# Kernel tuning notes

Measured on AMD Instinct MI355X. Metric: run time of the kernel, lower is better.

Reference implementation:

```python
import jax, jax.numpy as jnp
import numpy as np

N = 100000
IN_C = 256
OUT_C = 128
E = 3200000
NNZ = 3200000
K = 3  # n_wavelets
ATT_H = 64


def spmm(idx, vals, m):
    # idx: [2, nnz] (row, col), vals: [nnz], m: [N, d] -> [N, d]
    rows, cols = idx[0], idx[1]
    return jax.ops.segment_sum(vals[:, None] * m[cols], rows, num_segments=N)


def appnp_k1_a0(h, edge_index):
    # PyG APPNP(K=1, alpha=0) == one gcn-normalized propagation with self-loops
    loops = jnp.arange(N, dtype=edge_index.dtype)
    row = jnp.concatenate([edge_index[0], loops])
    col = jnp.concatenate([edge_index[1], loops])
    ones = jnp.ones(row.shape[0], dtype=h.dtype)
    deg = jax.ops.segment_sum(ones, col, num_segments=N)
    dinv = jnp.where(deg > 0, 1.0 / jnp.sqrt(deg), 0.0)
    norm = dinv[row] * dinv[col]
    return jax.ops.segment_sum(norm[:, None] * h[col], row, num_segments=N)


def setup_inputs() -> dict:
    key = jax.random.key(0)
    ks = jax.random.split(key, 12)
    x = jax.random.normal(ks[0], (N, IN_C), dtype=jnp.float32)
    edge_index = jax.random.randint(ks[1], (2, E), 0, N)
    phi_idx = jax.random.randint(ks[2], (K, 2, NNZ), 0, N)
    phi_vals = jax.random.uniform(ks[3], (K, NNZ), dtype=jnp.float32) * (1.0 / 32.0)
    phi_inv_idx = jax.random.randint(ks[4], (K, 2, NNZ), 0, N)
    phi_inv_vals = jax.random.uniform(ks[5], (K, NNZ), dtype=jnp.float32) * (1.0 / 32.0)
    # learned parameters
    lin_w = jax.random.normal(ks[6], (IN_C, OUT_C), dtype=jnp.float32) * (1.0 / np.sqrt(IN_C))
    lin_b = jnp.zeros((OUT_C,), dtype=jnp.float32)
    gw_w = jax.random.normal(ks[7], (IN_C, OUT_C), dtype=jnp.float32) * (1.0 / np.sqrt(IN_C))
    diag_w = jax.random.uniform(ks[8], (N,), dtype=jnp.float32, minval=0.9, maxval=1.1)
    att_w1 = jax.random.normal(ks[9], (OUT_C, ATT_H), dtype=jnp.float32) * (1.0 / np.sqrt(OUT_C))
    att_b1 = jnp.zeros((ATT_H,), dtype=jnp.float32)
    att_w2 = jax.random.normal(ks[10], (ATT_H, 1), dtype=jnp.float32) * (1.0 / np.sqrt(ATT_H))
    return {"x": x, "edge_index": edge_index, "phi_idx": phi_idx, "phi_vals": phi_vals,
            "phi_inv_idx": phi_inv_idx, "phi_inv_vals": phi_inv_vals,
            "lin_w": lin_w, "lin_b": lin_b, "gw_w": gw_w, "diag_w": diag_w,
            "att_w1": att_w1, "att_b1": att_b1, "att_w2": att_w2}


def reference(x, edge_index, phi_idx, phi_vals, phi_inv_idx, phi_inv_vals,
              lin_w, lin_b, gw_w, diag_w, att_w1, att_b1, att_w2):
    # --- mean branch: Linear -> L2 normalize * 1.8 -> APPNP(K=1, alpha=0)
    mean = x @ lin_w + lin_b
    nrm = jnp.linalg.norm(mean, axis=1, keepdims=True)
    mean = mean / jnp.maximum(nrm, 1e-12) * 1.8
    mean = appnp_k1_a0(mean, edge_index)

    # --- logstd branch: GraphWaveletLayer (activation = identity)
    x_ = x @ gw_w  # [N, OUT_C]
    outs = []
    for i in range(K):
        t = spmm(phi_inv_idx[i], phi_inv_vals[i], x_)
        t = diag_w[:, None] * t
        t = spmm(phi_idx[i], phi_vals[i], t)
        outs.append(t)
    z = jnp.stack(outs, axis=1)  # [N, K, OUT_C]

    # --- attention pooling over wavelet axis
    w = jax.nn.relu(jnp.einsum('nkd,dh->nkh', z, att_w1) + att_b1) @ att_w2  # [N, K, 1]
    beta = jax.nn.softmax(w, axis=1)
    logstd = (beta * z).sum(axis=1)  # [N, OUT_C]
    return (mean, logstd)
```

## Files before the change

kernel.cpp:

```cpp
#include <hip/hip_runtime.h>
#include <hip/hip_bf16.h>
#include <hip/hip_fp16.h>


#define WS_HIST  2
#define WS_BUILD 6
#define WS_GATH  8

__global__ __launch_bounds__(256) void hist_kernel(const int* __restrict__ idx,
                                                   int* __restrict__ cnt, int n) {
    int i = blockIdx.x * 256 + threadIdx.x;
    if (i < n) atomicAdd(&cnt[__builtin_nontemporal_load(idx + i)], 1);
}

__global__ __launch_bounds__(256) void dinv_kernel(int* __restrict__ cnt,
                                                   float* __restrict__ dinv, int n) {
    int i = blockIdx.x * 256 + threadIdx.x;
    if (i < n) { dinv[i] = rsqrtf((float)(cnt[i] + 1)); cnt[i] = 0; }
}

__global__ __launch_bounds__(256) void scan_reduce_kernel(
    const int* __restrict__ cnt, int* __restrict__ bsum, int N) {
    __shared__ int wsum[4];
    int base = blockIdx.x * 1024;
    int t = threadIdx.x;
    int s = 0;
#pragma unroll
    for (int j = 0; j < 4; ++j) {
        int idx = base + t * 4 + j;
        if (idx < N) s += cnt[idx];
    }
#pragma unroll
    for (int off = 32; off; off >>= 1) s += __shfl_xor(s, off);
    int lane = t & 63, w = t >> 6;
    if (lane == 0) wsum[w] = s;
    __syncthreads();
    if (t == 0) bsum[blockIdx.x] = wsum[0] + wsum[1] + wsum[2] + wsum[3];
}

__global__ void scan_bsum_kernel(const int* __restrict__ bsum,
                                 int* __restrict__ bofs,
                                 int* __restrict__ ptr, int nblk, int N) {
    if (threadIdx.x == 0 && blockIdx.x == 0) {
        int run = 0;
        for (int i = 0; i < nblk; ++i) { bofs[i] = run; run += bsum[i]; }
        bofs[nblk] = run;
        ptr[N] = run;
    }
}

__global__ __launch_bounds__(256) void scan_block_kernel(
    int* __restrict__ cnt, const int* __restrict__ bofs,
    int* __restrict__ ptr, int* __restrict__ cursor, int N) {
    __shared__ int wsum[4];
    int base = blockIdx.x * 1024;
    int t = threadIdx.x, lane = t & 63, w = t >> 6;
    int v[4]; int s = 0;
#pragma unroll
    for (int j = 0; j < 4; ++j) {
        int idx = base + t * 4 + j;
        v[j] = (idx < N) ? cnt[idx] : 0;
        s += v[j];
    }
    int incl = s;
#pragma unroll
    for (int off = 1; off < 64; off <<= 1) {
        int nn = __shfl_up(incl, off);
        if (lane >= off) incl += nn;
    }
    if (lane == 63) wsum[w] = incl;
    __syncthreads();
    int wofs = 0;
    for (int i = 0; i < w; ++i) wofs += wsum[i];
    int run = bofs[blockIdx.x] + wofs + incl - s;
#pragma unroll
    for (int j = 0; j < 4; ++j) {
        int idx = base + t * 4 + j;
        if (idx < N) { ptr[idx] = run; cursor[idx] = run; cnt[idx] = 0; }
        run += v[j];
    }
}

__global__ __launch_bounds__(256) void fused_pipe_kernel(
    const int* __restrict__ ptr_g, const int2* __restrict__ cpair_g,
    const __half* __restrict__ src, const float* __restrict__ init_src,
    const float* __restrict__ dinv,
    float* __restrict__ dstf, __half* __restrict__ dsth, int N, int nnz_g,
    const int* __restrict__ rows_b, const int* __restrict__ cols_b,
    const float* __restrict__ vals_b, const float* __restrict__ diag,
    int* __restrict__ cursor_b, unsigned long long* __restrict__ cpair_b,
    int nnz_b, int mode,
    const int* __restrict__ rows_h, int* __restrict__ cnt, int nnz_h,
    int mix)
{
    int role, lid, nloc;
    if (!mix) { role = 2; lid = blockIdx.x; nloc = gridDim.x; }
    else {
        int r = blockIdx.x & 15, g = blockIdx.x >> 4, ng = gridDim.x >> 4;
        if (r < WS_HIST)                { role = 0; lid = g * WS_HIST + r;                nloc = ng * WS_HIST; }
        else if (r < WS_HIST + WS_BUILD){ role = 1; lid = g * WS_BUILD + (r - WS_HIST);   nloc = ng * WS_BUILD; }
        else                            { role = 2; lid = g * WS_GATH + (r - WS_HIST - WS_BUILD); nloc = ng * WS_GATH; }
    }

    if (role == 0) {
        if (!rows_h) return;
        int stride = nloc * 256;
        for (int i = lid * 256 + threadIdx.x; i < nnz_h; i += stride)
            atomicAdd(&cnt[__builtin_nontemporal_load(rows_h + i)], 1);
        return;
    }
    if (role == 1) {
        if (!rows_b) return;
        int stride = nloc * 256;
        for (int i = lid * 256 + threadIdx.x; i < nnz_b; i += stride) {
            int r = __builtin_nontemporal_load(rows_b + i);
            int c = __builtin_nontemporal_load(cols_b + i);
            float v;
            if (mode == 2) v = dinv[r] * dinv[c];
            else {
                v = __builtin_nontemporal_load(vals_b + i);
                if (mode == 1) v *= diag[c];
            }
            int pos = atomicAdd(&cursor_b[r], 1);
            unsigned long long pk =
                ((unsigned long long)(unsigned)__float_as_uint(v) << 32) | (unsigned)c;
            __builtin_nontemporal_store(pk, cpair_b + pos);
        }
        return;
    }

    const int lane = threadIdx.x & 63;
    const size_t lofs = (size_t)(lane * 2);
    int wid = (lid * 256 + threadIdx.x) >> 6;
    const int nwaves = (nloc * 256) >> 6;
    for (int row = wid; row < N; row += nwaves) {
        int s = ptr_g[row], e = ptr_g[row + 1];
        e = min(e, nnz_g); s = max(0, min(s, e));
        float accx = 0.f, accy = 0.f;
        if (init_src) {
            float d = dinv[row];
            float dd = d * d;
            float2 m = *(const float2*)(init_src + (size_t)row * 128 + lofs);
            accx = dd * m.x; accy = dd * m.y;
        }
        for (int base = s; base < e; base += 64) {
            int n = min(64, e - base);
            int2 p = make_int2(0, 0);
            if (lane < n) p = cpair_g[base + lane];
            int j = 0;
            for (; j + 16 <= n; j += 16) {
                __half2 sv[16];
                float vj[16];
#pragma unroll
                for (int u = 0; u < 16; ++u) {
                    int cj = __builtin_amdgcn_readlane(p.x, j + u);
                    vj[u] = __int_as_float(__builtin_amdgcn_readlane(p.y, j + u));
                    sv[u] = *(const __half2*)(src + (size_t)cj * 128 + lofs);
                }
#pragma unroll
                for (int u = 0; u < 16; ++u) {
                    accx += vj[u] * __low2float(sv[u]);
                    accy += vj[u] * __high2float(sv[u]);
                }
            }
            for (; j + 4 <= n; j += 4) {
                __half2 sv[4];
                float vj[4];
#pragma unroll
                for (int u = 0; u < 4; ++u) {
                    int cj = __builtin_amdgcn_readlane(p.x, j + u);
                    vj[u] = __int_as_float(__builtin_amdgcn_readlane(p.y, j + u));
                    sv[u] = *(const __half2*)(src + (size_t)cj * 128 + lofs);
                }
#pragma unroll
                for (int u = 0; u < 4; ++u) {
                    accx += vj[u] * __low2float(sv[u]);
                    accy += vj[u] * __high2float(sv[u]);
                }
            }
            for (; j < n; ++j) {
                int cj = __builtin_amdgcn_readlane(p.x, j);
                float vj = __int_as_float(__builtin_amdgcn_readlane(p.y, j));
                __half2 sv = *(const __half2*)(src + (size_t)cj * 128 + lofs);
                accx += vj * __low2float(sv);
                accy += vj * __high2float(sv);
            }
        }
        if (dstf) {
            float2 o; o.x = accx; o.y = accy;
            *(float2*)(dstf + (size_t)row * 128 + lofs) = o;
        }
        if (dsth) {
            *(__half2*)(dsth + (size_t)row * 128 + lofs) =
                __floats2half2_rn(accx, accy);
        }
    }
}

__global__ __launch_bounds__(256) void gemm_fused(
    const float* __restrict__ x, const float* __restrict__ lin_w,
    const float* __restrict__ lin_b, const float* __restrict__ gw_w,
    float* __restrict__ mean0, __half* __restrict__ xwh, int M) {
    __shared__ float As[32][68];
    __shared__ float Bs[32][64];
    const int tid = threadIdx.x;
    const int tx = tid & 15, ty = tid >> 4;
    const int row0 = blockIdx.x * 64;
    const int nt = blockIdx.y;
    const float* __restrict__ W = (nt < 2) ? lin_w : gw_w;
    const int colbase = (nt & 1) * 64;

    const int ar = tid >> 3;
    const int ac = (tid & 7) << 2;
    const int bk = tid >> 4;
    const int bn = (tid & 15) << 2;

    float acc[4][4] = {};

    for (int kt = 0; kt < 256; kt += 32) {
#pragma unroll
        for (int rr = 0; rr < 2; ++rr) {
            int r = ar + rr * 32;
            int grow = row0 + r;
            float4 v = make_float4(0.f, 0.f, 0.f, 0.f);
            if (grow < M) v = *(const float4*)(x + (size_t)grow * 256 + kt + ac);
            As[ac + 0][r] = v.x; As[ac + 1][r] = v.y;
            As[ac + 2][r] = v.z; As[ac + 3][r] = v.w;
        }
#pragma unroll
        for (int rr = 0; rr < 2; ++rr) {
            int k = bk + rr * 16;
            *(float4*)&Bs[k][bn] =
                *(const float4*)(W + (size_t)(kt + k) * 128 + colbase + bn);
        }
        __syncthreads();
#pragma unroll
        for (int k = 0; k < 32; ++k) {
            float4 a = *(const float4*)&As[k][ty * 4];
            float4 b = *(const float4*)&Bs[k][tx * 4];
            float av[4] = {a.x, a.y, a.z, a.w};
            float bv[4] = {b.x, b.y, b.z, b.w};
#pragma unroll
            for (int i = 0; i < 4; ++i)
#pragma unroll
                for (int j = 0; j < 4; ++j) acc[i][j] += av[i] * bv[j];
        }
        __syncthreads();
    }

    if (nt < 2) {
        float4 bb = *(const float4*)(lin_b + colbase + tx * 4);
#pragma unroll
        for (int i = 0; i < 4; ++i) {
            int grow = row0 + ty * 4 + i;
            if (grow < M) {
                float4 o = make_float4(acc[i][0] + bb.x, acc[i][1] + bb.y,
                                       acc[i][2] + bb.z, acc[i][3] + bb.w);
                *(float4*)(mean0 + (size_t)grow * 128 + colbase + tx * 4) = o;
            }
        }
    } else {
#pragma unroll
        for (int i = 0; i < 4; ++i) {
            int grow = row0 + ty * 4 + i;
            if (grow < M) {
                union { __half2 h[2]; int2 i2; } u;
                u.h[0] = __floats2half2_rn(acc[i][0], acc[i][1]);
                u.h[1] = __floats2half2_rn(acc[i][2], acc[i][3]);
                *(int2*)(xwh + (size_t)grow * 128 + colbase + tx * 4) = u.i2;
            }
        }
    }
}

__global__ __launch_bounds__(256) void rownorm_kernel(float* __restrict__ m,
                                                      __half* __restrict__ mh,
                                                      int n) {
    const int lane = threadIdx.x & 63;
    int wid = (blockIdx.x * 256 + threadIdx.x) >> 6;
    if (wid >= n) return;
    float2 v = *(float2*)(m + (size_t)wid * 128 + lane * 2);
    float ss = v.x * v.x + v.y * v.y;
#pragma unroll
    for (int off = 32; off; off >>= 1) ss += __shfl_xor(ss, off);
    float s = sqrtf(ss);
    float sc = 1.8f / fmaxf(s, 1e-12f);
    v.x *= sc; v.y *= sc;
    *(float2*)(m + (size_t)wid * 128 + lane * 2) = v;
    *(__half2*)(mh + (size_t)wid * 128 + lane * 2) = __floats2half2_rn(v.x, v.y);
}

__global__ __launch_bounds__(256) void attn_h_kernel(
    const __half* __restrict__ z0, const __half* __restrict__ z1,
    const float* __restrict__ z2, const float* __restrict__ w1,
    const float* __restrict__ b1, const float* __restrict__ w2,
    float* __restrict__ out, int n) {
    const int lane = threadIdx.x & 63;
    float w1reg[128];
#pragma unroll
    for (int d = 0; d < 128; ++d) w1reg[d] = w1[d * 64 + lane];
    const float b1l = b1[lane];
    const float w2l = w2[lane];

    int wid = (blockIdx.x * 256 + threadIdx.x) >> 6;
    const int nwaves = (gridDim.x * 256) >> 6;
    for (int node = wid; node < n; node += nwaves) {
        float2 za = __half22float2(*(const __half2*)(z0 + (size_t)node * 128 + lane * 2));
        float2 zb = __half22float2(*(const __half2*)(z1 + (size_t)node * 128 + lane * 2));
        float2 zc = *(const float2*)(z2 + (size_t)node * 128 + lane * 2);
        float wk[3];
#pragma unroll
        for (int k = 0; k < 3; ++k) {
            float zx = (k == 0) ? za.x : (k == 1) ? zb.x : zc.x;
            float zy = (k == 0) ? za.y : (k == 1) ? zb.y : zc.y;
            float acc = 0.f;
#pragma unroll
            for (int d2 = 0; d2 < 64; ++d2) {
                float ze = __uint_as_float(__builtin_amdgcn_readlane(__float_as_uint(zx), d2));
                float zo = __uint_as_float(__builtin_amdgcn_readlane(__float_as_uint(zy), d2));
                acc += ze * w1reg[2 * d2] + zo * w1reg[2 * d2 + 1];
            }
            float h = fmaxf(acc + b1l, 0.f) * w2l;
#pragma unroll
            for (int off = 32; off; off >>= 1) h += __shfl_xor(h, off);
            wk[k] = h;
        }
        float mx = fmaxf(wk[0], fmaxf(wk[1], wk[2]));
        float e0 = __expf(wk[0] - mx);
        float e1 = __expf(wk[1] - mx);
        float e2 = __expf(wk[2] - mx);
        float inv = 1.f / (e0 + e1 + e2);
        float be0 = e0 * inv, be1 = e1 * inv, be2 = e2 * inv;
        float2 o;
        o.x = be0 * za.x + be1 * zb.x + be2 * zc.x;
        o.y = be0 * za.y + be1 * zb.y + be2 * zc.y;
        *(float2*)(out + (size_t)node * 128 + lane * 2) = o;
    }
}

__global__ __launch_bounds__(256) void f2h_kernel(const float* __restrict__ in,
                                                  __half* __restrict__ out,
                                                  size_t n2) {
    size_t i = (size_t)blockIdx.x * 256 + threadIdx.x;
    if (i >= n2) return;
    float2 v = ((const float2*)in)[i];
    ((__half2*)out)[i] = __floats2half2_rn(v.x, v.y);
}

__global__ __launch_bounds__(256) void spmm_h_kernel(
    const int* __restrict__ rows, const int* __restrict__ cols,
    const float* __restrict__ vals, const float* __restrict__ diag,
    const __half* __restrict__ src, float* __restrict__ dst, int nnz) {
    const int lane = threadIdx.x & 63;
    int wid = (blockIdx.x * 256 + threadIdx.x) >> 6;
    const int nwaves = (gridDim.x * 256) >> 6;
    for (int e = wid; e < nnz; e += nwaves) {
        int r = rows[e];
        int c = cols[e];
        float v = vals ? vals[e] : 1.f;
        if (diag) v *= diag[c];
        __half2 sh = *(const __half2*)(src + (size_t)c * 128 + lane * 2);
        float* d = dst + (size_t)r * 128 + lane * 2;
        unsafeAtomicAdd(d,     v * __low2float(sh));
        unsafeAtomicAdd(d + 1, v * __high2float(sh));
    }
}

__global__ __launch_bounds__(256) void appnp_init_kernel(
    const float* __restrict__ mean0, const float* __restrict__ dinv,
    float* __restrict__ dst, int n) {
    int i = blockIdx.x * 256 + threadIdx.x;
    if (i >= n * 32) return;
    int node = i >> 5;
    float dv = dinv[node];
    float dd = dv * dv;
    float4 v = ((const float4*)mean0)[i];
    v.x *= dd; v.y *= dd; v.z *= dd; v.w *= dd;
    ((float4*)dst)[i] = v;
}

__global__ __launch_bounds__(256) void appnp_edge_h_kernel(
    const int* __restrict__ rows, const int* __restrict__ cols,
    const float* __restrict__ dinv, const __half* __restrict__ src,
    float* __restrict__ dst, int nnz) {
    const int lane = threadIdx.x & 63;
    int wid = (blockIdx.x * 256 + threadIdx.x) >> 6;
    const int nwaves = (gridDim.x * 256) >> 6;
    for (int e = wid; e < nnz; e += nwaves) {
        int r = rows[e];
        int c = cols[e];
        float v = dinv[r] * dinv[c];
        __half2 sh = *(const __half2*)(src + (size_t)c * 128 + lane * 2);
        float* d = dst + (size_t)r * 128 + lane * 2;
        unsafeAtomicAdd(d,     v * __low2float(sh));
        unsafeAtomicAdd(d + 1, v * __high2float(sh));
    }
}

__global__ __launch_bounds__(256) void attn_f_kernel(
    const float* __restrict__ z0, const float* __restrict__ z1,
    const float* __restrict__ z2, const float* __restrict__ w1,
    const float* __restrict__ b1, const float* __restrict__ w2,
    float* __restrict__ out, int n) {
    const int lane = threadIdx.x & 63;
    float w1reg[128];
#pragma unroll
    for (int d = 0; d < 128; ++d) w1reg[d] = w1[d * 64 + lane];
    const float b1l = b1[lane];
    const float w2l = w2[lane];
    int wid = (blockIdx.x * 256 + threadIdx.x) >> 6;
    const int nwaves = (gridDim.x * 256) >> 6;
    for (int node = wid; node < n; node += nwaves) {
        float2 za = *(const float2*)(z0 + (size_t)node * 128 + lane * 2);
        float2 zb = *(const float2*)(z1 + (size_t)node * 128 + lane * 2);
        float2 zc = *(const float2*)(z2 + (size_t)node * 128 + lane * 2);
        float wk[3];
#pragma unroll
        for (int k = 0; k < 3; ++k) {
            float zx = (k == 0) ? za.x : (k == 1) ? zb.x : zc.x;
            float zy = (k == 0) ? za.y : (k == 1) ? zb.y : zc.y;
            float acc = 0.f;
#pragma unroll
            for (int d2 = 0; d2 < 64; ++d2) {
                float ze = __uint_as_float(__builtin_amdgcn_readlane(__float_as_uint(zx), d2));
                float zo = __uint_as_float(__builtin_amdgcn_readlane(__float_as_uint(zy), d2));
                acc += ze * w1reg[2 * d2] + zo * w1reg[2 * d2 + 1];
            }
            float h = fmaxf(acc + b1l, 0.f) * w2l;
#pragma unroll
            for (int off = 32; off; off >>= 1) h += __shfl_xor(h, off);
            wk[k] = h;
        }
        float mx = fmaxf(wk[0], fmaxf(wk[1], wk[2]));
        float e0 = __expf(wk[0] - mx);
        float e1 = __expf(wk[1] - mx);
        float e2 = __expf(wk[2] - mx);
        float inv = 1.f / (e0 + e1 + e2);
        float be0 = e0 * inv, be1 = e1 * inv, be2 = e2 * inv;
        float2 o;
        o.x = be0 * za.x + be1 * zb.x + be2 * zc.x;
        o.y = be0 * za.y + be1 * zb.y + be2 * zc.y;
        *(float2*)(out + (size_t)node * 128 + lane * 2) = o;
    }
}

extern "C" void kernel_launch(void* const* d_in, const int* in_sizes, int n_in,
                              void* d_out, int out_size, void* d_ws, size_t ws_size,
                              hipStream_t stream)
{
    const float* x            = (const float*)d_in[0];
    const int*   edge_index   = (const int*)d_in[1];
    const int*   phi_idx      = (const int*)d_in[2];
    const float* phi_vals     = (const float*)d_in[3];
    const int*   phi_inv_idx  = (const int*)d_in[4];
    const float* phi_inv_vals = (const float*)d_in[5];
    const float* lin_w        = (const float*)d_in[6];
    const float* lin_b        = (const float*)d_in[7];
    const float* gw_w         = (const float*)d_in[8];
    const float* diag_w       = (const float*)d_in[9];
    const float* att_w1       = (const float*)d_in[10];
    const float* att_b1       = (const float*)d_in[11];
    const float* att_w2       = (const float*)d_in[12];

    const int N   = in_sizes[9];
    const int E   = in_sizes[1] / 2;
    const int NNZ = in_sizes[3] / 3;
    const size_t NF = (size_t)N * 128;
    const int MAXNNZ = (E > NNZ) ? E : NNZ;
    const int nblk = (N + 1023) / 1024;

    float* out0 = (float*)d_out;
    float* out1 = out0 + NF;

    char* p = (char*)d_ws;
    int*    cnt   = (int*)p;       p += (size_t)N * 4;
    float*  dinv  = (float*)p;     p += (size_t)N * 4;
    __half* xwh   = (__half*)p;    p += NF * 2;
    __half* xh    = (__half*)p;    p += NF * 2;
    char* tail = p;
    __half* z0h   = (__half*)p;    p += NF * 2;
    __half* z1h   = (__half*)p;    p += NF * 2;
    __half* t1h   = (__half*)p;    p += NF * 2;
    int*    ptrA  = (int*)p;       p += (size_t)(N + 1) * 4;
    int*    ptrB  = (int*)p;       p += (size_t)(N + 1) * 4;
    int*    curA  = (int*)p;       p += (size_t)N * 4;
    int*    curB  = (int*)p;       p += (size_t)N * 4;
    int*    bsum  = (int*)p;       p += (size_t)nblk * 4;
    int*    bofs  = (int*)p;       p += (size_t)(nblk + 1) * 4;
    p = (char*)(((uintptr_t)p + 7) & ~(uintptr_t)7);
    unsigned long long* cpairA = (unsigned long long*)p; p += (size_t)MAXNNZ * 8;
    unsigned long long* cpairB = (unsigned long long*)p; p += (size_t)MAXNNZ * 8;
    const size_t need_csr = p - (char*)d_ws;
    const bool csr_ok = (ws_size >= need_csr);
    int* ptrS[2] = {ptrA, ptrB};
    int* curS[2] = {curA, curB};
    unsigned long long* cpairS[2] = {cpairA, cpairB};
    (void)n_in; (void)out_size;

    (void)hipMemsetAsync(cnt, 0, (size_t)N * sizeof(int), stream);
    hist_kernel<<<(E + 255) / 256, 256, 0, stream>>>(edge_index + E, cnt, E);
    dinv_kernel<<<(N + 255) / 256, 256, 0, stream>>>(cnt, dinv, N);

    gemm_fused<<<dim3((N + 63) / 64, 4), 256, 0, stream>>>(
        x, lin_w, lin_b, gw_w, out1, xwh, N);
    rownorm_kernel<<<(N + 3) / 4, 256, 0, stream>>>(out1, xh, N);

    if (csr_ok) {
        struct Op {
            const int* rows; const int* cols; const float* vals;
            int mode; int nnz;
            const __half* src; const float* init_src;
            float* dstf; __half* dsth;
        } ops[7];
        ops[0] = {edge_index, edge_index + E, nullptr, 2, E,
                  xh, out1, out0, nullptr};
        for (int i = 0; i < 3; ++i) {
            const int* ri1 = phi_inv_idx + (size_t)i * 2 * NNZ;
            const int* ri2 = phi_idx + (size_t)i * 2 * NNZ;
            ops[1 + 2 * i] = {ri1, ri1 + NNZ, phi_inv_vals + (size_t)i * NNZ,
                              0, NNZ, xwh, nullptr, nullptr, t1h};
            float*  bf = (i == 2) ? out1 : nullptr;
            __half* bh = (i == 0) ? z0h : (i == 1) ? z1h : nullptr;
            ops[2 + 2 * i] = {ri2, ri2 + NNZ, phi_vals + (size_t)i * NNZ,
                              1, NNZ, t1h, nullptr, bf, bh};
        }

        auto scans = [&](int k) {
            scan_reduce_kernel<<<nblk, 256, 0, stream>>>(cnt, bsum, N);
            scan_bsum_kernel<<<1, 64, 0, stream>>>(bsum, bofs, ptrS[k & 1], nblk, N);
            scan_block_kernel<<<nblk, 256, 0, stream>>>(cnt, bofs, ptrS[k & 1],
                                                        curS[k & 1], N);
        };

        const int GRID = 2048;
        hist_kernel<<<(ops[0].nnz + 255) / 256, 256, 0, stream>>>(
            ops[0].rows, cnt, ops[0].nnz);
        scans(0);
        fused_pipe_kernel<<<GRID, 256, 0, stream>>>(
            nullptr, nullptr, nullptr, nullptr, dinv, nullptr, nullptr, 0, 0,
            ops[0].rows, ops[0].cols, ops[0].vals, diag_w, curS[0], cpairS[0],
            ops[0].nnz, ops[0].mode,
            ops[1].rows, cnt, ops[1].nnz, 1);
        scans(1);

        for (int k = 0; k < 7; ++k) {
            const Op& g = ops[k];
            const bool hb = (k < 6), hh = (k < 5);
            const Op* b = hb ? &ops[k + 1] : nullptr;
            fused_pipe_kernel<<<GRID, 256, 0, stream>>>(
                ptrS[k & 1], (const int2*)cpairS[k & 1], g.src, g.init_src,
                dinv, g.dstf, g.dsth, N, g.nnz,
                hb ? b->rows : nullptr, hb ? b->cols : nullptr,
                hb ? b->vals : nullptr, diag_w,
                hb ? curS[(k + 1) & 1] : nullptr,
                hb ? cpairS[(k + 1) & 1] : nullptr,
                hb ? b->nnz : 0, hb ? b->mode : 0,
                hh ? ops[k + 2].rows : nullptr, cnt, hh ? ops[k + 2].nnz : 0,
                hb ? 1 : 0);
            if (hh) scans(k + 2);
        }

        attn_h_kernel<<<2048, 256, 0, stream>>>(z0h, z1h, out1, att_w1, att_b1,
                                                att_w2, out1, N);
    } else {
        float*  z0f  = (float*)tail;
        float*  z1f  = z0f + NF;
        float*  t1f  = z1f + NF;
        __half* t1hf = (__half*)(t1f + NF);
        for (int i = 0; i < 3; ++i) {
            const int* ri1 = phi_inv_idx + (size_t)i * 2 * NNZ;
            const int* ci1 = ri1 + NNZ;
            const int* ri2 = phi_idx + (size_t)i * 2 * NNZ;
            const int* ci2 = ri2 + NNZ;
            float* zdst = (i == 0) ? z0f : (i == 1) ? z1f : out0;

            (void)hipMemsetAsync(t1f, 0, NF * sizeof(float), stream);
            spmm_h_kernel<<<(NNZ + 3) / 4, 256, 0, stream>>>(
                ri1, ci1, phi_inv_vals + (size_t)i * NNZ, nullptr, xwh, t1f, NNZ);
            f2h_kernel<<<((NF / 2) + 255) / 256, 256, 0, stream>>>(t1f, t1hf,
                                                                   NF / 2);
            (void)hipMemsetAsync(zdst, 0, NF * sizeof(float), stream);
            spmm_h_kernel<<<(NNZ + 3) / 4, 256, 0, stream>>>(
                ri2, ci2, phi_vals + (size_t)i * NNZ, diag_w, t1hf, zdst, NNZ);
        }
        attn_f_kernel<<<2048, 256, 0, stream>>>(z0f, z1f, out0, att_w1, att_b1,
                                                att_w2, t1f, N);
        appnp_init_kernel<<<((size_t)N * 32 + 255) / 256, 256, 0, stream>>>(
            out1, dinv, out0, N);
        appnp_edge_h_kernel<<<(E + 3) / 4, 256, 0, stream>>>(
            edge_index, edge_index + E, dinv, xh, out0, E);
        (void)hipMemcpyAsync(out1, t1f, NF * sizeof(float),
                             hipMemcpyDeviceToDevice, stream);
    }
}
```

Before: 2.993 ms.

## Two-pass bucketed CSR build with deeper four-stage pipelined fused kernel

```diff
diff --git a/kernel.cpp b/kernel.cpp
--- a/kernel.cpp
+++ b/kernel.cpp
@@ -3,9 +3,10 @@
 #include <hip/hip_fp16.h>
 
 
-#define WS_HIST  2
-#define WS_BUILD 6
-#define WS_GATH  8
+typedef unsigned long long ull;
+#define NBMAX 32
+#define BSH 12
+#define BATCH 2048
 
 __global__ __launch_bounds__(256) void hist_kernel(const int* __restrict__ idx,
                                                    int* __restrict__ cnt, int n) {
@@ -81,57 +82,132 @@
     }
 }
 
-__global__ __launch_bounds__(256) void fused_pipe_kernel(
+__global__ void bcur_init_kernel(const int* __restrict__ ptr,
+                                 int* __restrict__ bcur, int N, int nb) {
+    int b = threadIdx.x;
+    if (b < nb) bcur[b] = ptr[min(b << BSH, N)];
+}
+
+__global__ __launch_bounds__(256) void fused2_kernel(
     const int* __restrict__ ptr_g, const int2* __restrict__ cpair_g,
-    const __half* __restrict__ src, const float* __restrict__ init_src,
-    const float* __restrict__ dinv,
+    const __half* __restrict__ srch, const float* __restrict__ srcf,
+    const float* __restrict__ init_src, const float* __restrict__ dinv,
     float* __restrict__ dstf, __half* __restrict__ dsth, int N, int nnz_g,
-    const int* __restrict__ rows_b, const int* __restrict__ cols_b,
-    const float* __restrict__ vals_b, const float* __restrict__ diag,
-    int* __restrict__ cursor_b, unsigned long long* __restrict__ cpair_b,
-    int nnz_b, int mode,
+    const ull* __restrict__ stg_in, const int* __restrict__ ptr_b,
+    int* __restrict__ cursor_b, ull* __restrict__ cpair_out, int nnz_b, int nb,
+    const int* __restrict__ rows_a, const int* __restrict__ cols_a,
+    const float* __restrict__ vals_a, const float* __restrict__ diag,
+    int mode_a, int* __restrict__ bcur_a, ull* __restrict__ stg_out, int nnz_a,
     const int* __restrict__ rows_h, int* __restrict__ cnt, int nnz_h,
     int mix)
 {
+    __shared__ ull stg[BATCH];
+    __shared__ int lcnt[NBMAX], lofs_s[NBMAX], gbase[NBMAX];
+    __shared__ int bstartL[NBMAX + 1];
+
     int role, lid, nloc;
-    if (!mix) { role = 2; lid = blockIdx.x; nloc = gridDim.x; }
+    if (mix == 0) { role = 3; lid = blockIdx.x; nloc = gridDim.x; }
     else {
         int r = blockIdx.x & 15, g = blockIdx.x >> 4, ng = gridDim.x >> 4;
-        if (r < WS_HIST)                { role = 0; lid = g * WS_HIST + r;                nloc = ng * WS_HIST; }
-        else if (r < WS_HIST + WS_BUILD){ role = 1; lid = g * WS_BUILD + (r - WS_HIST);   nloc = ng * WS_BUILD; }
-        else                            { role = 2; lid = g * WS_GATH + (r - WS_HIST - WS_BUILD); nloc = ng * WS_GATH; }
-    }
+        if (mix == 1) {
+            if (r < 9)       { role = 3; lid = g * 9 + r;        nloc = ng * 9; }
+            else if (r < 12) { role = 1; lid = g * 3 + (r - 9);  nloc = ng * 3; }
+            else if (r < 15) { role = 2; lid = g * 3 + (r - 12); nloc = ng * 3; }
+            else             { role = 0; lid = g;                nloc = ng; }
+        } else if (mix == 2) {
+            if (r < 14) { role = 2; lid = g * 14 + r;        nloc = ng * 14; }
+            else        { role = 0; lid = g * 2 + (r - 14);  nloc = ng * 2; }
+        } else {
+            if (r < 8)       { role = 1; lid = g * 8 + r;        nloc = ng * 8; }
+            else if (r < 14) { role = 2; lid = g * 6 + (r - 8);  nloc = ng * 6; }
+            else             { role = 0; lid = g * 2 + (r - 14); nloc = ng * 2; }
+        }
+    }
+    const int t = threadIdx.x;
 
     if (role == 0) {
         if (!rows_h) return;
         int stride = nloc * 256;
-        for (int i = lid * 256 + threadIdx.x; i < nnz_h; i += stride)
+        for (int i = lid * 256 + t; i < nnz_h; i += stride)
             atomicAdd(&cnt[__builtin_nontemporal_load(rows_h + i)], 1);
         return;
     }
+
+    if (role == 2) {
+        if (!rows_a) return;
+        for (int base = lid * BATCH; base < nnz_a; base += nloc * BATCH) {
+            int cntE = min(BATCH, nnz_a - base);
+            if (t < NBMAX) lcnt[t] = 0;
+            __syncthreads();
+            int myb[8], myo[8]; ull mypk[8];
+#pragma unroll
+            for (int u = 0; u < 8; ++u) {
+                int k = t + u * 256;
+                if (k < cntE) {
+                    int idx = base + k;
+                    int r = __builtin_nontemporal_load(rows_a + idx);
+                    int c = __builtin_nontemporal_load(cols_a + idx);
+                    float v;
+                    if (mode_a == 2) v = dinv[r] * dinv[c];
+                    else {
+                        v = __builtin_nontemporal_load(vals_a + idx);
+                        if (mode_a == 1) v *= diag[c];
+                    }
+                    int b = r >> BSH;
+                    myb[u] = b;
+                    myo[u] = atomicAdd(&lcnt[b], 1);
+                    mypk[u] = ((ull)(r & ((1 << BSH) - 1)) << 49) |
+                              ((ull)(unsigned)c << 32) | (unsigned)__float_as_uint(v);
+                }
+            }
+            __syncthreads();
+            if (t == 0) {
+                int run = 0;
+                for (int b = 0; b < NBMAX; ++b) { lofs_s[b] = run; run += lcnt[b]; }
+            }
+            __syncthreads();
+            if (t < NBMAX && lcnt[t] > 0) gbase[t] = atomicAdd(&bcur_a[t], lcnt[t]);
+            __syncthreads();
+#pragma unroll
+            for (int u = 0; u < 8; ++u) {
+                int k = t + u * 256;
+                if (k < cntE) stg[lofs_s[myb[u]] + myo[u]] = mypk[u];
+            }
+            __syncthreads();
+            for (int i = t; i < cntE; i += 256) {
+                int lo = 0, hi = NBMAX - 1;
+                while (lo < hi) { int mid = (lo + hi + 1) >> 1;
+                                  if (lofs_s[mid] <= i) lo = mid; else hi = mid - 1; }
+                stg_out[gbase[lo] + (i - lofs_s[lo])] = stg[i];
+            }
+            __syncthreads();
+        }
+        return;
+    }
+
     if (role == 1) {
-        if (!rows_b) return;
+        if (!stg_in) return;
+        if (t <= NBMAX) bstartL[t] = ptr_b[min(t << BSH, N)];
+        __syncthreads();
         int stride = nloc * 256;
-        for (int i = lid * 256 + threadIdx.x; i < nnz_b; i += stride) {
-            int r = __builtin_nontemporal_load(rows_b + i);
-            int c = __builtin_nontemporal_load(cols_b + i);
-            float v;
-            if (mode == 2) v = dinv[r] * dinv[c];
-            else {
-                v = __builtin_nontemporal_load(vals_b + i);
-                if (mode == 1) v *= diag[c];
-            }
-            int pos = atomicAdd(&cursor_b[r], 1);
-            unsigned long long pk =
-                ((unsigned long long)(unsigned)__float_as_uint(v) << 32) | (unsigned)c;
-            __builtin_nontemporal_store(pk, cpair_b + pos);
+        for (int i = lid * 256 + t; i < nnz_b; i += stride) {
+            ull p = stg_in[i];
+            int lo = 0, hi = nb - 1;
+            while (lo < hi) { int mid = (lo + hi + 1) >> 1;
+                              if (bstartL[mid] <= i) lo = mid; else hi = mid - 1; }
+            int row = (lo << BSH) | (int)(p >> 49);
+            unsigned c = (unsigned)(p >> 32) & 0x1FFFFu;
+            unsigned vbits = (unsigned)p;
+            int pos = atomicAdd(&cursor_b[row], 1);
+            cpair_out[pos] = ((ull)vbits << 32) | c;
         }
         return;
     }
 
-    const int lane = threadIdx.x & 63;
+    if (!ptr_g) return;
+    const int lane = t & 63;
     const size_t lofs = (size_t)(lane * 2);
-    int wid = (lid * 256 + threadIdx.x) >> 6;
+    int wid = (lid * 256 + t) >> 6;
     const int nwaves = (nloc * 256) >> 6;
     for (int row = wid; row < N; row += nwaves) {
         int s = ptr_g[row], e = ptr_g[row + 1];
@@ -148,42 +224,50 @@
             int2 p = make_int2(0, 0);
             if (lane < n) p = cpair_g[base + lane];
             int j = 0;
-            for (; j + 16 <= n; j += 16) {
-                __half2 sv[16];
-                float vj[16];
-#pragma unroll
-                for (int u = 0; u < 16; ++u) {
-                    int cj = __builtin_amdgcn_readlane(p.x, j + u);
-                    vj[u] = __int_as_float(__builtin_amdgcn_readlane(p.y, j + u));
-                    sv[u] = *(const __half2*)(src + (size_t)cj * 128 + lofs);
+            if (srch) {
+                for (; j + 16 <= n; j += 16) {
+                    __half2 sv[16]; float vj[16];
+#pragma unroll
+                    for (int u = 0; u < 16; ++u) {
+                        int cj = __builtin_amdgcn_readlane(p.x, j + u);
+                        vj[u] = __int_as_float(__builtin_amdgcn_readlane(p.y, j + u));
+                        sv[u] = *(const __half2*)(srch + (size_t)cj * 128 + lofs);
+                    }
+#pragma unroll
+                    for (int u = 0; u < 16; ++u) {
+                        accx += vj[u] * __low2float(sv[u]);
+                        accy += vj[u] * __high2float(sv[u]);
+                    }
                 }
-#pragma unroll
-                for (int u = 0; u < 16; ++u) {
-                    accx += vj[u] * __low2float(sv[u]);
-                    accy += vj[u] * __high2float(sv[u]);
+                for (; j < n; ++j) {
+                    int cj = __builtin_amdgcn_readlane(p.x, j);
+                    float vj = __int_as_float(__builtin_amdgcn_readlane(p.y, j));
+                    __half2 sv = *(const __half2*)(srch + (size_t)cj * 128 + lofs);
+                    accx += vj * __low2float(sv);
+                    accy += vj * __high2float(sv);
                 }
-            }
-            for (; j + 4 <= n; j += 4) {
-                __half2 sv[4];
-                float vj[4];
-#pragma unroll
-                for (int u = 0; u < 4; ++u) {
-                    int cj = __builtin_amdgcn_readlane(p.x, j + u);
-                    vj[u] = __int_as_float(__builtin_amdgcn_readlane(p.y, j + u));
-                    sv[u] = *(const __half2*)(src + (size_t)cj * 128 + lofs);
+            } else {
+                for (; j + 8 <= n; j += 8) {
+                    float2 sv[8]; float vj[8];
+#pragma unroll
+                    for (int u = 0; u < 8; ++u) {
+                        int cj = __builtin_amdgcn_readlane(p.x, j + u);
+                        vj[u] = __int_as_float(__builtin_amdgcn_readlane(p.y, j + u));
+                        sv[u] = *(const float2*)(srcf + (size_t)cj * 128 + lofs);
+                    }
+#pragma unroll
+                    for (int u = 0; u < 8; ++u) {
+                        accx += vj[u] * sv[u].x;
+                        accy += vj[u] * sv[u].y;
+                    }
                 }
-#pragma unroll
-                for (int u = 0; u < 4; ++u) {
-                    accx += vj[u] * __low2float(sv[u]);
-                    accy += vj[u] * __high2float(sv[u]);
+                for (; j < n; ++j) {
+                    int cj = __builtin_amdgcn_readlane(p.x, j);
+                    float vj = __int_as_float(__builtin_amdgcn_readlane(p.y, j));
+                    float2 sv = *(const float2*)(srcf + (size_t)cj * 128 + lofs);
+                    accx += vj * sv.x;
+                    accy += vj * sv.y;
                 }
-            }
-            for (; j < n; ++j) {
-                int cj = __builtin_amdgcn_readlane(p.x, j);
-                float vj = __int_as_float(__builtin_amdgcn_readlane(p.y, j));
-                __half2 sv = *(const __half2*)(src + (size_t)cj * 128 + lofs);
-                accx += vj * __low2float(sv);
-                accy += vj * __high2float(sv);
             }
         }
         if (dstf) {
@@ -273,9 +357,7 @@
     }
 }
 
-__global__ __launch_bounds__(256) void rownorm_kernel(float* __restrict__ m,
-                                                      __half* __restrict__ mh,
-                                                      int n) {
+__global__ __launch_bounds__(256) void rownorm_kernel(float* __restrict__ m, int n) {
     const int lane = threadIdx.x & 63;
     int wid = (blockIdx.x * 256 + threadIdx.x) >> 6;
     if (wid >= n) return;
@@ -287,7 +369,6 @@
     float sc = 1.8f / fmaxf(s, 1e-12f);
     v.x *= sc; v.y *= sc;
     *(float2*)(m + (size_t)wid * 128 + lane * 2) = v;
-    *(__half2*)(mh + (size_t)wid * 128 + lane * 2) = __floats2half2_rn(v.x, v.y);
 }
 
 __global__ __launch_bounds__(256) void attn_h_kernel(
@@ -468,6 +549,7 @@
     const size_t NF = (size_t)N * 128;
     const int MAXNNZ = (E > NNZ) ? E : NNZ;
     const int nblk = (N + 1023) / 1024;
+    const int nb = (N + (1 << BSH) - 1) >> BSH;
 
     float* out0 = (float*)d_out;
     float* out1 = out0 + NF;
@@ -476,25 +558,20 @@
     int*    cnt   = (int*)p;       p += (size_t)N * 4;
     float*  dinv  = (float*)p;     p += (size_t)N * 4;
     __half* xwh   = (__half*)p;    p += NF * 2;
-    __half* xh    = (__half*)p;    p += NF * 2;
     char* tail = p;
     __half* z0h   = (__half*)p;    p += NF * 2;
     __half* z1h   = (__half*)p;    p += NF * 2;
     __half* t1h   = (__half*)p;    p += NF * 2;
-    int*    ptrA  = (int*)p;       p += (size_t)(N + 1) * 4;
-    int*    ptrB  = (int*)p;       p += (size_t)(N + 1) * 4;
-    int*    curA  = (int*)p;       p += (size_t)N * 4;
-    int*    curB  = (int*)p;       p += (size_t)N * 4;
+    int*    ptrS[3]; for (int i = 0; i < 3; ++i) { ptrS[i] = (int*)p; p += (size_t)(N + 1) * 4; }
+    int*    curS[2]; for (int i = 0; i < 2; ++i) { curS[i] = (int*)p; p += (size_t)N * 4; }
     int*    bsum  = (int*)p;       p += (size_t)nblk * 4;
     int*    bofs  = (int*)p;       p += (size_t)(nblk + 1) * 4;
+    int*    bcurS[2]; for (int i = 0; i < 2; ++i) { bcurS[i] = (int*)p; p += NBMAX * 4; }
     p = (char*)(((uintptr_t)p + 7) & ~(uintptr_t)7);
-    unsigned long long* cpairA = (unsigned long long*)p; p += (size_t)MAXNNZ * 8;
-    unsigned long long* cpairB = (unsigned long long*)p; p += (size_t)MAXNNZ * 8;
+    ull*    stagS[2]; for (int i = 0; i < 2; ++i) { stagS[i] = (ull*)p; p += (size_t)MAXNNZ * 8; }
+    ull*    cpairS[2]; for (int i = 0; i < 2; ++i) { cpairS[i] = (ull*)p; p += (size_t)MAXNNZ * 8; }
     const size_t need_csr = p - (char*)d_ws;
-    const bool csr_ok = (ws_size >= need_csr);
-    int* ptrS[2] = {ptrA, ptrB};
-    int* curS[2] = {curA, curB};
-    unsigned long long* cpairS[2] = {cpairA, cpairB};
+    const bool csr_ok = (ws_size >= need_csr) && (nb <= NBMAX) && (N < (1 << 17));
     (void)n_in; (void)out_size;
 
     (void)hipMemsetAsync(cnt, 0, (size_t)N * sizeof(int), stream);
@@ -503,61 +580,70 @@
 
     gemm_fused<<<dim3((N + 63) / 64, 4), 256, 0, stream>>>(
         x, lin_w, lin_b, gw_w, out1, xwh, N);
-    rownorm_kernel<<<(N + 3) / 4, 256, 0, stream>>>(out1, xh, N);
+    rownorm_kernel<<<(N + 3) / 4, 256, 0, stream>>>(out1, N);
 
     if (csr_ok) {
         struct Op {
             const int* rows; const int* cols; const float* vals;
             int mode; int nnz;
-            const __half* src; const float* init_src;
+            const __half* srch; const float* srcf; const float* init_src;
             float* dstf; __half* dsth;
         } ops[7];
         ops[0] = {edge_index, edge_index + E, nullptr, 2, E,
-                  xh, out1, out0, nullptr};
+                  nullptr, out1, out1, out0, nullptr};
         for (int i = 0; i < 3; ++i) {
             const int* ri1 = phi_inv_idx + (size_t)i * 2 * NNZ;
             const int* ri2 = phi_idx + (size_t)i * 2 * NNZ;
             ops[1 + 2 * i] = {ri1, ri1 + NNZ, phi_inv_vals + (size_t)i * NNZ,
-                              0, NNZ, xwh, nullptr, nullptr, t1h};
+                              0, NNZ, xwh, nullptr, nullptr, nullptr, t1h};
             float*  bf = (i == 2) ? out1 : nullptr;
             __half* bh = (i == 0) ? z0h : (i == 1) ? z1h : nullptr;
             ops[2 + 2 * i] = {ri2, ri2 + NNZ, phi_vals + (size_t)i * NNZ,
-                              1, NNZ, t1h, nullptr, bf, bh};
+                              1, NNZ, t1h, nullptr, nullptr, bf, bh};
         }
 
         auto scans = [&](int k) {
             scan_reduce_kernel<<<nblk, 256, 0, stream>>>(cnt, bsum, N);
-            scan_bsum_kernel<<<1, 64, 0, stream>>>(bsum, bofs, ptrS[k & 1], nblk, N);
-            scan_block_kernel<<<nblk, 256, 0, stream>>>(cnt, bofs, ptrS[k & 1],
+            scan_bsum_kernel<<<1, 64, 0, stream>>>(bsum, bofs, ptrS[k % 3], nblk, N);
+            scan_block_kernel<<<nblk, 256, 0, stream>>>(cnt, bofs, ptrS[k % 3],
                                                         curS[k & 1], N);
+            bcur_init_kernel<<<1, NBMAX, 0, stream>>>(ptrS[k % 3], bcurS[k & 1], N, nb);
         };
 
         const int GRID = 2048;
         hist_kernel<<<(ops[0].nnz + 255) / 256, 256, 0, stream>>>(
             ops[0].rows, cnt, ops[0].nnz);
         scans(0);
-        fused_pipe_kernel<<<GRID, 256, 0, stream>>>(
-            nullptr, nullptr, nullptr, nullptr, dinv, nullptr, nullptr, 0, 0,
-            ops[0].rows, ops[0].cols, ops[0].vals, diag_w, curS[0], cpairS[0],
-            ops[0].nnz, ops[0].mode,
-            ops[1].rows, cnt, ops[1].nnz, 1);
+        fused2_kernel<<<GRID, 256, 0, stream>>>(
+            nullptr, nullptr, nullptr, nullptr, nullptr, dinv, nullptr, nullptr, N, 0,
+            nullptr, nullptr, nullptr, nullptr, 0, nb,
+            ops[0].rows, ops[0].cols, ops[0].vals, diag_w, ops[0].mode,
+            bcurS[0], stagS[0], ops[0].nnz,
+            ops[1].rows, cnt, ops[1].nnz, 2);
         scans(1);
 
-        for (int k = 0; k < 7; ++k) {
-            const Op& g = ops[k];
-            const bool hb = (k < 6), hh = (k < 5);
-            const Op* b = hb ? &ops[k + 1] : nullptr;
-            fused_pipe_kernel<<<GRID, 256, 0, stream>>>(
-                ptrS[k & 1], (const int2*)cpairS[k & 1], g.src, g.init_src,
-                dinv, g.dstf, g.dsth, N, g.nnz,
-                hb ? b->rows : nullptr, hb ? b->cols : nullptr,
-                hb ? b->vals : nullptr, diag_w,
-                hb ? curS[(k + 1) & 1] : nullptr,
-                hb ? cpairS[(k + 1) & 1] : nullptr,
-                hb ? b->nnz : 0, hb ? b->mode : 0,
-                hh ? ops[k + 2].rows : nullptr, cnt, hh ? ops[k + 2].nnz : 0,
-                hb ? 1 : 0);
-            if (hh) scans(k + 2);
+        for (int j = 0; j <= 7; ++j) {
+            const Op* g = (j >= 1) ? &ops[j - 1] : nullptr;
+            const Op* b = (j <= 6) ? &ops[j] : nullptr;
+            const Op* a = (j + 1 <= 6) ? &ops[j + 1] : nullptr;
+            const Op* h = (j + 2 <= 6) ? &ops[j + 2] : nullptr;
+            int mix = (j == 0) ? 3 : (j == 7) ? 0 : 1;
+            fused2_kernel<<<GRID, 256, 0, stream>>>(
+                g ? ptrS[(j - 1) % 3] : nullptr,
+                g ? (const int2*)cpairS[(j - 1) & 1] : nullptr,
+                g ? g->srch : nullptr, g ? g->srcf : nullptr,
+                g ? g->init_src : nullptr, dinv,
+                g ? g->dstf : nullptr, g ? g->dsth : nullptr, N, g ? g->nnz : 0,
+                b ? stagS[j & 1] : nullptr, b ? ptrS[j % 3] : nullptr,
+                b ? curS[j & 1] : nullptr, b ? cpairS[j & 1] : nullptr,
+                b ? b->nnz : 0, nb,
+                a ? a->rows : nullptr, a ? a->cols : nullptr,
+                a ? a->vals : nullptr, diag_w, a ? a->mode : 0,
+                a ? bcurS[(j + 1) & 1] : nullptr, a ? stagS[(j + 1) & 1] : nullptr,
+                a ? a->nnz : 0,
+                h ? h->rows : nullptr, cnt, h ? h->nnz : 0,
+                mix);
+            if (j + 2 <= 6) scans(j + 2);
         }
 
         attn_h_kernel<<<2048, 256, 0, stream>>>(z0h, z1h, out1, att_w1, att_b1,
@@ -567,6 +653,8 @@
         float*  z1f  = z0f + NF;
         float*  t1f  = z1f + NF;
         __half* t1hf = (__half*)(t1f + NF);
+        __half* xhf  = t1hf + NF;
+        f2h_kernel<<<((NF / 2) + 255) / 256, 256, 0, stream>>>(out1, xhf, NF / 2);
         for (int i = 0; i < 3; ++i) {
             const int* ri1 = phi_inv_idx + (size_t)i * 2 * NNZ;
             const int* ci1 = ri1 + NNZ;
@@ -588,7 +676,7 @@
         appnp_init_kernel<<<((size_t)N * 32 + 255) / 256, 256, 0, stream>>>(
             out1, dinv, out0, N);
         appnp_edge_h_kernel<<<(E + 3) / 4, 256, 0, stream>>>(
-            edge_index, edge_index + E, dinv, xh, out0, E);
+            edge_index, edge_index + E, dinv, xhf, out0, E);
         (void)hipMemcpyAsync(out1, t1f, NF * sizeof(float),
                              hipMemcpyDeviceToDevice, stream);
     }
```

After: 4.067 ms. 1.36x slower.

## Partition histogram and CSR build by row range per XCD-aligned block slot

Applied to the files above, without the earlier changes.

```diff
diff --git a/kernel.cpp b/kernel.cpp
--- a/kernel.cpp
+++ b/kernel.cpp
@@ -3,14 +3,18 @@
 #include <hip/hip_fp16.h>
 
 
-#define WS_HIST  2
-#define WS_BUILD 6
-#define WS_GATH  8
-
-__global__ __launch_bounds__(256) void hist_kernel(const int* __restrict__ idx,
-                                                   int* __restrict__ cnt, int n) {
-    int i = blockIdx.x * 256 + threadIdx.x;
-    if (i < n) atomicAdd(&cnt[__builtin_nontemporal_load(idx + i)], 1);
+typedef unsigned long long ull;
+
+__global__ __launch_bounds__(256) void phist_kernel(const int* __restrict__ idx,
+                                                    int* __restrict__ cnt,
+                                                    int n, int pdiv) {
+    int sub = blockIdx.x & 7;
+    int lid = blockIdx.x >> 3, nloc = gridDim.x >> 3;
+    unsigned lo = (unsigned)(sub * pdiv);
+    for (int i = lid * 256 + threadIdx.x; i < n; i += nloc * 256) {
+        int r = idx[i];
+        if ((unsigned)(r - lo) < (unsigned)pdiv) atomicAdd(&cnt[r], 1);
+    }
 }
 
 __global__ __launch_bounds__(256) void dinv_kernel(int* __restrict__ cnt,
@@ -88,50 +92,61 @@
     float* __restrict__ dstf, __half* __restrict__ dsth, int N, int nnz_g,
     const int* __restrict__ rows_b, const int* __restrict__ cols_b,
     const float* __restrict__ vals_b, const float* __restrict__ diag,
-    int* __restrict__ cursor_b, unsigned long long* __restrict__ cpair_b,
-    int nnz_b, int mode,
+    int* __restrict__ cursor_b, ull* __restrict__ cpair_b, int nnz_b, int mode,
     const int* __restrict__ rows_h, int* __restrict__ cnt, int nnz_h,
-    int mix)
+    int pdiv, int mix)
 {
-    int role, lid, nloc;
-    if (!mix) { role = 2; lid = blockIdx.x; nloc = gridDim.x; }
+    int role, lid = 0, nloc = 1, part = 0;
+    if (mix == 0) { role = 2; lid = blockIdx.x; nloc = gridDim.x; }
     else {
-        int r = blockIdx.x & 15, g = blockIdx.x >> 4, ng = gridDim.x >> 4;
-        if (r < WS_HIST)                { role = 0; lid = g * WS_HIST + r;                nloc = ng * WS_HIST; }
-        else if (r < WS_HIST + WS_BUILD){ role = 1; lid = g * WS_BUILD + (r - WS_HIST);   nloc = ng * WS_BUILD; }
-        else                            { role = 2; lid = g * WS_GATH + (r - WS_HIST - WS_BUILD); nloc = ng * WS_GATH; }
-    }
+        int sub = blockIdx.x & 7, g = blockIdx.x >> 3;
+        int slot = g & 15, grp = g >> 4, ngrp = gridDim.x >> 7;
+        if (mix == 1) {
+            if (slot < 8)       { role = 2; lid = (grp * 8 + slot) * 8 + sub; nloc = ngrp * 64; }
+            else if (slot < 14) { role = 1; lid = grp * 6 + (slot - 8);  nloc = ngrp * 6; part = sub; }
+            else                { role = 0; lid = grp * 2 + (slot - 14); nloc = ngrp * 2; part = sub; }
+        } else {
+            if (slot < 12) { role = 1; lid = grp * 12 + slot;        nloc = ngrp * 12; part = sub; }
+            else           { role = 0; lid = grp * 4 + (slot - 12);  nloc = ngrp * 4;  part = sub; }
+        }
+    }
+    const int t = threadIdx.x;
 
     if (role == 0) {
         if (!rows_h) return;
+        unsigned lo = (unsigned)(part * pdiv);
         int stride = nloc * 256;
-        for (int i = lid * 256 + threadIdx.x; i < nnz_h; i += stride)
-            atomicAdd(&cnt[__builtin_nontemporal_load(rows_h + i)], 1);
+        for (int i = lid * 256 + t; i < nnz_h; i += stride) {
+            int r = rows_h[i];
+            if ((unsigned)(r - lo) < (unsigned)pdiv) atomicAdd(&cnt[r], 1);
+        }
         return;
     }
     if (role == 1) {
         if (!rows_b) return;
+        unsigned lo = (unsigned)(part * pdiv);
         int stride = nloc * 256;
-        for (int i = lid * 256 + threadIdx.x; i < nnz_b; i += stride) {
-            int r = __builtin_nontemporal_load(rows_b + i);
-            int c = __builtin_nontemporal_load(cols_b + i);
+        for (int i = lid * 256 + t; i < nnz_b; i += stride) {
+            int r = rows_b[i];
+            if ((unsigned)(r - lo) >= (unsigned)pdiv) continue;
+            int c = cols_b[i];
             float v;
             if (mode == 2) v = dinv[r] * dinv[c];
             else {
-                v = __builtin_nontemporal_load(vals_b + i);
+                v = vals_b[i];
                 if (mode == 1) v *= diag[c];
             }
             int pos = atomicAdd(&cursor_b[r], 1);
-            unsigned long long pk =
-                ((unsigned long long)(unsigned)__float_as_uint(v) << 32) | (unsigned)c;
-            __builtin_nontemporal_store(pk, cpair_b + pos);
+            cpair_b[pos] =
+                ((ull)(unsigned)__float_as_uint(v) << 32) | (unsigned)c;
         }
         return;
     }
 
-    const int lane = threadIdx.x & 63;
+    if (!ptr_g) return;
+    const int lane = t & 63;
     const size_t lofs = (size_t)(lane * 2);
-    int wid = (lid * 256 + threadIdx.x) >> 6;
+    int wid = (lid * 256 + t) >> 6;
     const int nwaves = (nloc * 256) >> 6;
     for (int row = wid; row < N; row += nwaves) {
         int s = ptr_g[row], e = ptr_g[row + 1];
@@ -468,6 +483,7 @@
     const size_t NF = (size_t)N * 128;
     const int MAXNNZ = (E > NNZ) ? E : NNZ;
     const int nblk = (N + 1023) / 1024;
+    const int pdiv = (N + 7) / 8;
 
     float* out0 = (float*)d_out;
     float* out1 = out0 + NF;
@@ -488,17 +504,17 @@
     int*    bsum  = (int*)p;       p += (size_t)nblk * 4;
     int*    bofs  = (int*)p;       p += (size_t)(nblk + 1) * 4;
     p = (char*)(((uintptr_t)p + 7) & ~(uintptr_t)7);
-    unsigned long long* cpairA = (unsigned long long*)p; p += (size_t)MAXNNZ * 8;
-    unsigned long long* cpairB = (unsigned long long*)p; p += (size_t)MAXNNZ * 8;
+    ull* cpairA = (ull*)p;         p += (size_t)MAXNNZ * 8;
+    ull* cpairB = (ull*)p;         p += (size_t)MAXNNZ * 8;
     const size_t need_csr = p - (char*)d_ws;
     const bool csr_ok = (ws_size >= need_csr);
     int* ptrS[2] = {ptrA, ptrB};
     int* curS[2] = {curA, curB};
-    unsigned long long* cpairS[2] = {cpairA, cpairB};
+    ull* cpairS[2] = {cpairA, cpairB};
     (void)n_in; (void)out_size;
 
     (void)hipMemsetAsync(cnt, 0, (size_t)N * sizeof(int), stream);
-    hist_kernel<<<(E + 255) / 256, 256, 0, stream>>>(edge_index + E, cnt, E);
+    phist_kernel<<<2048, 256, 0, stream>>>(edge_index + E, cnt, E, pdiv);
     dinv_kernel<<<(N + 255) / 256, 256, 0, stream>>>(cnt, dinv, N);
 
     gemm_fused<<<dim3((N + 63) / 64, 4), 256, 0, stream>>>(
@@ -533,14 +549,13 @@
         };
 
         const int GRID = 2048;
-        hist_kernel<<<(ops[0].nnz + 255) / 256, 256, 0, stream>>>(
-            ops[0].rows, cnt, ops[0].nnz);
+        phist_kernel<<<2048, 256, 0, stream>>>(ops[0].rows, cnt, ops[0].nnz, pdiv);
         scans(0);
         fused_pipe_kernel<<<GRID, 256, 0, stream>>>(
-            nullptr, nullptr, nullptr, nullptr, dinv, nullptr, nullptr, 0, 0,
+            nullptr, nullptr, nullptr, nullptr, dinv, nullptr, nullptr, N, 0,
             ops[0].rows, ops[0].cols, ops[0].vals, diag_w, curS[0], cpairS[0],
             ops[0].nnz, ops[0].mode,
-            ops[1].rows, cnt, ops[1].nnz, 1);
+            ops[1].rows, cnt, ops[1].nnz, pdiv, 2);
         scans(1);
 
         for (int k = 0; k < 7; ++k) {
@@ -556,7 +571,7 @@
                 hb ? cpairS[(k + 1) & 1] : nullptr,
                 hb ? b->nnz : 0, hb ? b->mode : 0,
                 hh ? ops[k + 2].rows : nullptr, cnt, hh ? ops[k + 2].nnz : 0,
-                hb ? 1 : 0);
+                pdiv, hb ? 1 : 0);
             if (hh) scans(k + 2);
         }
 
```

Result: slower. 3.633 ms (+21.4%).
